# Kernel tuning notes

Hardware: AMD Instinct MI355X
Metric: run time of the kernel (lower is better)

## Reference

```python
import jax, jax.numpy as jnp
import numpy as np

B, L = 256, 8192
DIM, NPAT, HIST, WIN = 256, 64, 32, 8


def setup_inputs() -> dict:
    key = jax.random.key(0)
    ks = jax.random.split(key, 6)
    return {
        "x": jax.random.normal(ks[0], (B, L), dtype=jnp.float32),
        "avg_init": jax.random.normal(ks[1], (B, NPAT), dtype=jnp.float32),
        "conv_w": jax.random.normal(ks[2], (DIM, 1, HIST), dtype=jnp.float32) * 0.1,
        "conv_b": jax.random.normal(ks[3], (DIM,), dtype=jnp.float32) * 0.1,
        "keys_w": jax.random.normal(ks[4], (NPAT, DIM), dtype=jnp.float32) * 0.1,
        "shapes_w": jax.random.normal(ks[5], (WIN, NPAT), dtype=jnp.float32) * 0.1,
    }


def reference(x, avg_init, conv_w, conv_b, keys_w, shapes_w):
    b, l = x.shape
    n_pat = keys_w.shape[0]
    hist = conv_w.shape[2]
    win = shapes_w.shape[0]

    # randn avg_scores, centered (module draws fresh randn each forward; we take it as input)
    avg0 = avg_init - jnp.mean(avg_init, axis=-1, keepdims=True)

    padded = jnp.pad(x, ((0, 0), (hist - 1, 0)))[:, None, :]  # [B,1,L+hist-1]
    out = jax.lax.conv_general_dilated(
        padded, conv_w, window_strides=(win,), padding="VALID",
        dimension_numbers=("NCH", "OIH", "NCH"))
    out = out + conv_b[None, :, None]                     # [B,dim,T]
    out = jnp.transpose(out, (2, 0, 1))                   # [T,B,dim]

    # relu6(keys(out)) -> attn scores [T,B,n_pat]
    scores = jnp.clip(jnp.einsum("tbd,pd->tbp", out, keys_w), 0.0, 6.0)

    # sequential balanced-routing scan over T with running average scores
    def step(avg, score):                                 # avg,score: [B,n_pat]
        idx = jnp.argmax(score - avg, axis=-1)
        prob = jax.nn.one_hot(idx, n_pat, dtype=score.dtype)
        return avg + prob - 1.0 / n_pat, prob

    _, probs = jax.lax.scan(step, avg0, scores)           # probs: [T,B,n_pat]
    probs = jnp.transpose(probs, (1, 0, 2))               # [B,T,n_pat]

    signal = jnp.einsum("btp,wp->btw", probs, shapes_w).reshape(b, -1)[:, :l]
    return jax.nn.relu(signal - x)
```

## Files before the change

kernel.cpp:

```cpp
#include <hip/hip_runtime.h>


constexpr int Bb = 256, Ll = 8192, DIMc = 256, NPAT = 64, HIST = 32, WINc = 8;
constexpr int Tt = Ll / WINc;
constexpr int TC = 32;
constexpr int NC = Tt / TC;
constexpr float CINV = 1.0f / 64.0f;

#define DPP_MAXF(m, ctrl, rmask)                                               \
  do {                                                                         \
    int _mi = __float_as_int(m);                                               \
    int _ti = __builtin_amdgcn_update_dpp(_mi, _mi, (ctrl), (rmask), 0xF, false); \
    (m) = fmaxf((m), __int_as_float(_ti));                                     \
  } while (0)

__global__ __launch_bounds__(256) void precompute_kernel(
    const float* __restrict__ conv_w, const float* __restrict__ conv_b,
    const float* __restrict__ keys_w, float* __restrict__ wsf) {
  __shared__ float part[8][32];
  __shared__ float bred[4];
  const int p = blockIdx.x;
  const int t = threadIdx.x;
  const int h = t & 31, g = t >> 5;
  const float* kwp = keys_w + (size_t)p * DIMc;

  float acc = 0.f;
#pragma unroll
  for (int dd = 0; dd < 32; ++dd) {
    int d = g * 32 + dd;
    acc = fmaf(kwp[d], conv_w[d * HIST + h], acc);
  }
  part[g][h] = acc;

  float bp = kwp[t] * conv_b[t];
#pragma unroll
  for (int off = 32; off; off >>= 1) bp += __shfl_down(bp, off);
  if ((t & 63) == 0) bred[t >> 6] = bp;
  __syncthreads();

  if (t < 32) {
    float s = 0.f;
#pragma unroll
    for (int gg = 0; gg < 8; ++gg) s += part[gg][t];
    wsf[(t >> 2) * (NPAT * 4) + p * 4 + (t & 3)] = s;
  } else if (t == 32) {
    wsf[NPAT * HIST + p] = (bred[0] + bred[1]) + (bred[2] + bred[3]);
  }
}

__global__ __launch_bounds__(256) void shaper_kernel(
    const float* __restrict__ x, const float* __restrict__ avg_init,
    const float* __restrict__ shapes_w, const float* __restrict__ wsf,
    float* __restrict__ out) {
  __shared__ __align__(16) float xpad[HIST - 1 + Ll + 1];
  __shared__ float scb[2][TC * NPAT];
  __shared__ int   idxb[Tt];
  __shared__ float shp[WINc * NPAT];

  const int b    = blockIdx.x;
  const int tid  = threadIdx.x;
  const int wid  = tid >> 6;
  const int lane = tid & 63;
  const float* xrow = x + (size_t)b * Ll;

  if (tid < HIST - 1) xpad[tid] = 0.f;
  {
    const float4* xv4 = (const float4*)xrow;
#pragma unroll
    for (int k = 0; k < 8; ++k) {
      int i4 = k * 256 + tid;
      float4 v = xv4[i4];
      float* dst = xpad + HIST - 1 + i4 * 4;
      dst[0] = v.x; dst[1] = v.y; dst[2] = v.z; dst[3] = v.w;
    }
  }
  for (int i = tid; i < WINc * NPAT; i += 256) shp[i] = shapes_w[i];

  float4 w2v[8];
  float  b2 = 0.f;
  if (wid > 0) {
    const float4* w2g = (const float4*)wsf;
#pragma unroll
    for (int h4 = 0; h4 < 8; ++h4) w2v[h4] = w2g[h4 * 64 + lane];
    b2 = wsf[NPAT * HIST + lane];
  }
  float av = 0.f;
  if (wid == 0) {
    const float* ai = avg_init + (size_t)b * NPAT;
    float s = 0.f;
    for (int j = 0; j < NPAT; ++j) s += ai[j];
    av = ai[lane] - s * (1.0f / NPAT);
  }
  __syncthreads();

  auto fill = [&](int c, float* __restrict__ sb) {
    int base = c * TC;
    for (int tl = wid - 1; tl < TC; tl += 3) {
      int t = base + tl;
      const float4* xw = (const float4*)(xpad + t * WINc);
      float acc = b2;
#pragma unroll
      for (int h4 = 0; h4 < 8; ++h4) {
        float4 xv = xw[h4];
        float4 wv = w2v[h4];
        acc = fmaf(xv.x, wv.x, acc);
        acc = fmaf(xv.y, wv.y, acc);
        acc = fmaf(xv.z, wv.z, acc);
        acc = fmaf(xv.w, wv.w, acc);
      }
      sb[tl * NPAT + lane] = fminf(fmaxf(acc, 0.f), 6.f);
    }
  };

  auto scan_chunk = [&](const float* __restrict__ sb, int tbase) {
    float r[TC];
#pragma unroll
    for (int i = 0; i < TC; ++i) r[i] = sb[i * NPAT + lane];
    float v = r[0] - av;
    int stash = 0;
#pragma unroll
    for (int i = 0; i < TC; ++i) {
      float t0 = av - CINV;
      float t1 = (av + 1.0f) - CINV;
      float vA = 0.f, vB = 0.f;
      if (i + 1 < TC) { vA = r[i + 1] - t0; vB = r[i + 1] - t1; }
      float m = v;
      DPP_MAXF(m, 0xB1, 0xF);
      DPP_MAXF(m, 0x4E, 0xF);
      DPP_MAXF(m, 0x141, 0xF);
      DPP_MAXF(m, 0x140, 0xF);
      DPP_MAXF(m, 0x142, 0xA);
      DPP_MAXF(m, 0x143, 0xC);
      float gmax = __int_as_float(
          __builtin_amdgcn_readlane(__float_as_int(m), 63));
      unsigned long long mk = __ballot(v == gmax);
      int winner = __ffsll(mk) - 1;
      stash = (lane == i) ? winner : stash;
      bool win = (lane == winner);
      av = win ? t1 : t0;
      if (i + 1 < TC) v = win ? vB : vA;
    }
    if (lane < TC) idxb[tbase + lane] = stash;
  };

  if (wid > 0) fill(0, scb[0]);
  __syncthreads();

  for (int c = 0; c < NC; ++c) {
    if (wid == 0) {
      scan_chunk(scb[c & 1], c * TC);
    } else if (c + 1 < NC) {
      fill(c + 1, scb[(c + 1) & 1]);
    }
    __syncthreads();
  }

  float4* outv = (float4*)(out + (size_t)b * Ll);
#pragma unroll
  for (int k = 0; k < 8; ++k) {
    int i4 = k * 256 + tid;
    int l0 = i4 * 4;
    int t  = l0 >> 3;
    int w0 = l0 & 7;
    int p  = idxb[t];
    float4 o;
    o.x = fmaxf(shp[(w0 + 0) * NPAT + p] - xpad[HIST - 1 + l0 + 0], 0.f);
    o.y = fmaxf(shp[(w0 + 1) * NPAT + p] - xpad[HIST - 1 + l0 + 1], 0.f);
    o.z = fmaxf(shp[(w0 + 2) * NPAT + p] - xpad[HIST - 1 + l0 + 2], 0.f);
    o.w = fmaxf(shp[(w0 + 3) * NPAT + p] - xpad[HIST - 1 + l0 + 3], 0.f);
    outv[i4] = o;
  }
}

extern "C" void kernel_launch(void* const* d_in, const int* in_sizes, int n_in,
                              void* d_out, int out_size, void* d_ws, size_t ws_size,
                              hipStream_t stream) {
  const float* x        = (const float*)d_in[0];
  const float* avg_init = (const float*)d_in[1];
  const float* conv_w   = (const float*)d_in[2];
  const float* conv_b   = (const float*)d_in[3];
  const float* keys_w   = (const float*)d_in[4];
  const float* shapes_w = (const float*)d_in[5];
  float* wsf = (float*)d_ws;

  precompute_kernel<<<NPAT, 256, 0, stream>>>(conv_w, conv_b, keys_w, wsf);
  shaper_kernel<<<Bb, 256, 0, stream>>>(x, avg_init, shapes_w, wsf,
                                        (float*)d_out);
}
```

Measured before the change: 186.7 us.

## Restructure routing scan with ordered-int keys and deferred winner selection

Converts the per-step argmax in the sequential routing scan to unsigned order-preserving integer keys and keeps two candidate keys per lane, one for the not-winner case and one for the previous winner. The max reduction now excludes the previous winner's lane, stops after the row-level DPP stages and combines four readlanes with scalar max. The winner's alternative key is fetched separately, which takes the argmax off the critical dependency chain that previously waited on the full cross-row reduction. It adds scalar readlanes and tie-break logic and must preserve exact first-index tie semantics.

```diff
diff --git a/kernel.cpp b/kernel.cpp
--- a/kernel.cpp
+++ b/kernel.cpp
@@ -7,11 +7,16 @@
 constexpr int NC = Tt / TC;
 constexpr float CINV = 1.0f / 64.0f;
 
-#define DPP_MAXF(m, ctrl, rmask)                                               \
+__device__ __forceinline__ unsigned ordkey(float v) {
+  int b = __float_as_int(v);
+  return (unsigned)(b ^ ((b >> 31) | 0x80000000));
+}
+
+#define DPP_MAXU(m, ctrl)                                                      \
   do {                                                                         \
-    int _mi = __float_as_int(m);                                               \
-    int _ti = __builtin_amdgcn_update_dpp(_mi, _mi, (ctrl), (rmask), 0xF, false); \
-    (m) = fmaxf((m), __int_as_float(_ti));                                     \
+    unsigned _t = (unsigned)__builtin_amdgcn_update_dpp(                       \
+        (int)(m), (int)(m), (ctrl), 0xF, 0xF, false);                          \
+    (m) = ((m) > _t) ? (m) : _t;                                               \
   } while (0)
 
 __global__ __launch_bounds__(256) void precompute_kernel(
@@ -84,12 +89,12 @@
     for (int h4 = 0; h4 < 8; ++h4) w2v[h4] = w2g[h4 * 64 + lane];
     b2 = wsf[NPAT * HIST + lane];
   }
-  float av = 0.f;
+  float av0 = 0.f;
   if (wid == 0) {
     const float* ai = avg_init + (size_t)b * NPAT;
     float s = 0.f;
     for (int j = 0; j < NPAT; ++j) s += ai[j];
-    av = ai[lane] - s * (1.0f / NPAT);
+    av0 = ai[lane] - s * (1.0f / NPAT);
   }
   __syncthreads();
 
@@ -112,33 +117,46 @@
     }
   };
 
+  int   wS = 64;
+  float t0 = av0, t1 = av0;
+
   auto scan_chunk = [&](const float* __restrict__ sb, int tbase) {
     float r[TC];
 #pragma unroll
     for (int i = 0; i < TC; ++i) r[i] = sb[i * NPAT + lane];
-    float v = r[0] - av;
+    unsigned keyA = ordkey(r[0] - t0);
+    unsigned keyB = ordkey(r[0] - t1);
     int stash = 0;
 #pragma unroll
     for (int i = 0; i < TC; ++i) {
-      float t0 = av - CINV;
-      float t1 = (av + 1.0f) - CINV;
-      float vA = 0.f, vB = 0.f;
-      if (i + 1 < TC) { vA = r[i + 1] - t0; vB = r[i + 1] - t1; }
-      float m = v;
-      DPP_MAXF(m, 0xB1, 0xF);
-      DPP_MAXF(m, 0x4E, 0xF);
-      DPP_MAXF(m, 0x141, 0xF);
-      DPP_MAXF(m, 0x140, 0xF);
-      DPP_MAXF(m, 0x142, 0xA);
-      DPP_MAXF(m, 0x143, 0xC);
-      float gmax = __int_as_float(
-          __builtin_amdgcn_readlane(__float_as_int(m), 63));
-      unsigned long long mk = __ballot(v == gmax);
-      int winner = __ffsll(mk) - 1;
-      stash = (lane == i) ? winner : stash;
-      bool win = (lane == winner);
-      av = win ? t1 : t0;
-      if (i + 1 < TC) v = win ? vB : vA;
+      bool isw = (lane == wS);
+      unsigned keym0 = isw ? 0u : keyA;
+      unsigned m = keym0;
+      DPP_MAXU(m, 0xB1);
+      DPP_MAXU(m, 0x4E);
+      DPP_MAXU(m, 0x141);
+      DPP_MAXU(m, 0x140);
+      unsigned m0 = (unsigned)__builtin_amdgcn_readlane((int)m, 15);
+      unsigned m1 = (unsigned)__builtin_amdgcn_readlane((int)m, 31);
+      unsigned m2 = (unsigned)__builtin_amdgcn_readlane((int)m, 47);
+      unsigned m3 = (unsigned)__builtin_amdgcn_readlane((int)m, 63);
+      unsigned ka = m0 > m1 ? m0 : m1;
+      unsigned kb = m2 > m3 ? m2 : m3;
+      unsigned K1 = ka > kb ? ka : kb;
+      unsigned KB = (unsigned)__builtin_amdgcn_readlane((int)keyB, wS);
+      unsigned long long bal = __ballot(keym0 == K1);
+      int I1 = __ffsll(bal) - 1;
+      int wnew = (KB > K1) ? wS : ((KB == K1) ? (wS < I1 ? wS : I1) : I1);
+
+      float av = isw ? t1 : t0;
+      t0 = av - CINV;
+      t1 = (av + 1.0f) - CINV;
+      if (i + 1 < TC) {
+        keyA = ordkey(r[i + 1] - t0);
+        keyB = ordkey(r[i + 1] - t1);
+      }
+      stash = (lane == i) ? wnew : stash;
+      wS = wnew;
     }
     if (lane < TC) idxb[tbase + lane] = stash;
   };
```

After: 202.6 us. +8.5%, slower.

## Restructure routing scan with top-2 lookahead to shorten serial argmax dependency

Applied to the files above, without the earlier changes.

Scores are pre-shifted by the initial average and a time-dependent constant, so the scan only tracks an integer count per lane. Each step computes a top-2 reduction over ordered-int keys plus ballot masks that do not depend on the previous step's winner. The winner is then resolved with cheap scalar bit logic on the previous winner, taking the cross-lane reduction off the serial critical path. Winners are packed into 64-bit scalar registers, and the per-row mean of avg_init is computed with a DPP reduction instead of a serial loop. Rewriting the float arithmetic this way risks small rounding differences in tie-breaking.

```diff
diff --git a/kernel.cpp b/kernel.cpp
--- a/kernel.cpp
+++ b/kernel.cpp
@@ -7,12 +7,34 @@
 constexpr int NC = Tt / TC;
 constexpr float CINV = 1.0f / 64.0f;
 
-#define DPP_MAXF(m, ctrl, rmask)                                               \
+__device__ __forceinline__ unsigned ordk(float v) {
+  int b = __float_as_int(v);
+  return (unsigned)(b ^ ((b >> 31) | 0x80000000));
+}
+
+#define DPPI(x, ctrl) \
+  ((unsigned)__builtin_amdgcn_update_dpp((int)(x), (int)(x), (ctrl), 0xF, 0xF, false))
+
+#define TOP2_STAGE(M, S, ctrl)                    \
+  do {                                            \
+    unsigned _Md = DPPI(M, ctrl);                 \
+    unsigned _Sd = DPPI(S, ctrl);                 \
+    unsigned _mn = (M) < _Md ? (M) : _Md;         \
+    (M) = (M) > _Md ? (M) : _Md;                  \
+    (S) = (S) > _Sd ? (S) : _Sd;                  \
+    (S) = (S) > _mn ? (S) : _mn;                  \
+  } while (0)
+
+#define DPP_ADDF(s, ctrl, rmask)                                               \
   do {                                                                         \
-    int _mi = __float_as_int(m);                                               \
-    int _ti = __builtin_amdgcn_update_dpp(_mi, _mi, (ctrl), (rmask), 0xF, false); \
-    (m) = fmaxf((m), __int_as_float(_ti));                                     \
+    int _si = __float_as_int(s);                                               \
+    int _ti = __builtin_amdgcn_update_dpp(_si, _si, (ctrl), (rmask), 0xF, false); \
+    (s) += __int_as_float(_ti);                                                \
   } while (0)
+
+struct BalSet {
+  unsigned long long E1, E2, GT, GE;
+};
 
 __global__ __launch_bounds__(256) void precompute_kernel(
     const float* __restrict__ conv_w, const float* __restrict__ conv_b,
@@ -76,6 +98,20 @@
   }
   for (int i = tid; i < WINc * NPAT; i += 256) shp[i] = shapes_w[i];
 
+  float av0 = 0.f;
+  {
+    float s = avg_init[(size_t)b * NPAT + lane];
+    float t = s;
+    DPP_ADDF(t, 0xB1, 0xF);
+    DPP_ADDF(t, 0x4E, 0xF);
+    DPP_ADDF(t, 0x141, 0xF);
+    DPP_ADDF(t, 0x140, 0xF);
+    DPP_ADDF(t, 0x142, 0xA);
+    DPP_ADDF(t, 0x143, 0xC);
+    float tot = __int_as_float(__builtin_amdgcn_readlane(__float_as_int(t), 63));
+    av0 = s - tot * CINV;
+  }
+
   float4 w2v[8];
   float  b2 = 0.f;
   if (wid > 0) {
@@ -83,13 +119,6 @@
 #pragma unroll
     for (int h4 = 0; h4 < 8; ++h4) w2v[h4] = w2g[h4 * 64 + lane];
     b2 = wsf[NPAT * HIST + lane];
-  }
-  float av = 0.f;
-  if (wid == 0) {
-    const float* ai = avg_init + (size_t)b * NPAT;
-    float s = 0.f;
-    for (int j = 0; j < NPAT; ++j) s += ai[j];
-    av = ai[lane] - s * (1.0f / NPAT);
   }
   __syncthreads();
 
@@ -108,39 +137,87 @@
         acc = fmaf(xv.z, wv.z, acc);
         acc = fmaf(xv.w, wv.w, acc);
       }
-      sb[tl * NPAT + lane] = fminf(fmaxf(acc, 0.f), 6.f);
-    }
+      float sc = fminf(fmaxf(acc, 0.f), 6.f);
+      sb[tl * NPAT + lane] = (sc - av0) + (float)t * CINV;
+    }
+  };
+
+  float cnt = 0.f;
+  int   wp  = -1;
+  unsigned long long m_w = 0;
+  const float vone = 1.0f;
+
+  auto mkb = [&](float zv) {
+    BalSet B;
+    float z1 = zv - vone;
+    unsigned zu = ordk(zv);
+    unsigned M = zu, S = 0u;
+    TOP2_STAGE(M, S, 0xB1);
+    TOP2_STAGE(M, S, 0x4E);
+    TOP2_STAGE(M, S, 0x141);
+    TOP2_STAGE(M, S, 0x140);
+    unsigned M0 = (unsigned)__builtin_amdgcn_readlane((int)M, 0);
+    unsigned M1 = (unsigned)__builtin_amdgcn_readlane((int)M, 16);
+    unsigned M2 = (unsigned)__builtin_amdgcn_readlane((int)M, 32);
+    unsigned M3 = (unsigned)__builtin_amdgcn_readlane((int)M, 48);
+    unsigned S0 = (unsigned)__builtin_amdgcn_readlane((int)S, 0);
+    unsigned S1 = (unsigned)__builtin_amdgcn_readlane((int)S, 16);
+    unsigned S2 = (unsigned)__builtin_amdgcn_readlane((int)S, 32);
+    unsigned S3 = (unsigned)__builtin_amdgcn_readlane((int)S, 48);
+    unsigned h1 = M0 > M1 ? M0 : M1, l1 = M0 < M1 ? M0 : M1;
+    unsigned h2 = M2 > M3 ? M2 : M3, l2 = M2 < M3 ? M2 : M3;
+    unsigned Mu = h1 > h2 ? h1 : h2;
+    unsigned sa = h1 < h2 ? h1 : h2;
+    unsigned sb_ = l1 > l2 ? l1 : l2;
+    unsigned secM = sa > sb_ ? sa : sb_;
+    unsigned sr = S0 > S1 ? S0 : S1;
+    unsigned sr2 = S2 > S3 ? S2 : S3;
+    unsigned Smax = sr > sr2 ? sr : sr2;
+    unsigned Su = Smax > secM ? Smax : secM;
+    unsigned sbits = (Su >= 0x80000000u) ? (Su ^ 0x80000000u) : ~Su;
+    float Sf = __int_as_float((int)sbits);
+    B.E1 = __ballot(zu == Mu);
+    B.E2 = __ballot(zu == Su);
+    B.GT = __ballot(z1 > Sf);
+    B.GE = __ballot(z1 >= Sf);
+    return B;
   };
 
   auto scan_chunk = [&](const float* __restrict__ sb, int tbase) {
     float r[TC];
 #pragma unroll
     for (int i = 0; i < TC; ++i) r[i] = sb[i * NPAT + lane];
-    float v = r[0] - av;
-    int stash = 0;
+    unsigned long long sa0 = 0, sa1 = 0, sa2 = 0, sa3 = 0;
+    BalSet B = mkb(r[0] - cnt);
 #pragma unroll
     for (int i = 0; i < TC; ++i) {
-      float t0 = av - CINV;
-      float t1 = (av + 1.0f) - CINV;
-      float vA = 0.f, vB = 0.f;
-      if (i + 1 < TC) { vA = r[i + 1] - t0; vB = r[i + 1] - t1; }
-      float m = v;
-      DPP_MAXF(m, 0xB1, 0xF);
-      DPP_MAXF(m, 0x4E, 0xF);
-      DPP_MAXF(m, 0x141, 0xF);
-      DPP_MAXF(m, 0x140, 0xF);
-      DPP_MAXF(m, 0x142, 0xA);
-      DPP_MAXF(m, 0x143, 0xC);
-      float gmax = __int_as_float(
-          __builtin_amdgcn_readlane(__float_as_int(m), 63));
-      unsigned long long mk = __ballot(v == gmax);
-      int winner = __ffsll(mk) - 1;
-      stash = (lane == i) ? winner : stash;
-      bool win = (lane == winner);
-      av = win ? t1 : t0;
-      if (i + 1 < TC) v = win ? vB : vA;
-    }
-    if (lane < TC) idxb[tbase + lane] = stash;
+      unsigned long long b1x = B.E1 & ~m_w;
+      int jA  = __ffsll(b1x) - 1;
+      int jB1 = __ffsll(B.E2) - 1;
+      int wq  = wp & 63;
+      int gt  = (int)((B.GT >> wq) & 1);
+      int ge  = (int)((B.GE >> wq) & 1);
+      int jmn = wp < jB1 ? wp : jB1;
+      int wB  = gt ? wp : (ge ? jmn : jB1);
+      int w   = b1x ? jA : wB;
+      if (i < 10)      sa0 |= (unsigned long long)w << (6 * i);
+      else if (i < 20) sa1 |= (unsigned long long)w << (6 * (i - 10));
+      else if (i < 30) sa2 |= (unsigned long long)w << (6 * (i - 20));
+      else             sa3 |= (unsigned long long)w << (6 * (i - 30));
+      cnt += (lane == wp) ? 1.0f : 0.0f;
+      wp  = w;
+      m_w = 1ull << w;
+      if (i + 1 < TC) B = mkb(r[i + 1] - cnt);
+    }
+    cnt += (lane == wp) ? 1.0f : 0.0f;
+    wp  = -1;
+    m_w = 0;
+    unsigned long long src = (lane < 10) ? sa0 : (lane < 20) ? sa1
+                           : (lane < 30) ? sa2 : sa3;
+    int sh = 6 * (lane - ((lane < 10) ? 0 : (lane < 20) ? 10
+                          : (lane < 30) ? 20 : 30));
+    int widx = (int)((src >> sh) & 63);
+    if (lane < TC) idxb[tbase + lane] = widx;
   };
 
   if (wid > 0) fill(0, scb[0]);
```

Measured after the change: 261.8 us. 1.4x slower.

## Pack four patterns per lane in routing scan to shorten the argmax reduction

Applied to the files above, without the earlier changes.

The sequential routing scan now maps the 64 patterns onto 16 lanes with 4 patterns each, replicated across the four 16-lane rows. Each step does a local 4-way max plus 4 row-local DPP steps, which removes the cross-row DPP stages and the readlane from the serial critical path. The winner index is recovered from four ballots and a min, and the next chunk's score rows are prefetched as float4 loads in a rotating 3-register buffer. In exchange it adds extra ballots and selects per step. Exact ties would now mark several patterns as winners in the average update, which differs from the reference's first-index argmax.

```diff
diff --git a/kernel.cpp b/kernel.cpp
--- a/kernel.cpp
+++ b/kernel.cpp
@@ -7,10 +7,10 @@
 constexpr int NC = Tt / TC;
 constexpr float CINV = 1.0f / 64.0f;
 
-#define DPP_MAXF(m, ctrl, rmask)                                               \
+#define DPP_MAXF(m, ctrl)                                                      \
   do {                                                                         \
     int _mi = __float_as_int(m);                                               \
-    int _ti = __builtin_amdgcn_update_dpp(_mi, _mi, (ctrl), (rmask), 0xF, false); \
+    int _ti = __builtin_amdgcn_update_dpp(_mi, _mi, (ctrl), 0xF, 0xF, false);  \
     (m) = fmaxf((m), __int_as_float(_ti));                                     \
   } while (0)
 
@@ -53,7 +53,7 @@
     const float* __restrict__ shapes_w, const float* __restrict__ wsf,
     float* __restrict__ out) {
   __shared__ __align__(16) float xpad[HIST - 1 + Ll + 1];
-  __shared__ float scb[2][TC * NPAT];
+  __shared__ __align__(16) float scb[2][TC * NPAT];
   __shared__ int   idxb[Tt];
   __shared__ float shp[WINc * NPAT];
 
@@ -61,6 +61,7 @@
   const int tid  = threadIdx.x;
   const int wid  = tid >> 6;
   const int lane = tid & 63;
+  const int lq   = lane & 15;
   const float* xrow = x + (size_t)b * Ll;
 
   if (tid < HIST - 1) xpad[tid] = 0.f;
@@ -84,12 +85,14 @@
     for (int h4 = 0; h4 < 8; ++h4) w2v[h4] = w2g[h4 * 64 + lane];
     b2 = wsf[NPAT * HIST + lane];
   }
-  float av = 0.f;
+  float av[4] = {0.f, 0.f, 0.f, 0.f};
   if (wid == 0) {
     const float* ai = avg_init + (size_t)b * NPAT;
     float s = 0.f;
     for (int j = 0; j < NPAT; ++j) s += ai[j];
-    av = ai[lane] - s * (1.0f / NPAT);
+#pragma unroll
+    for (int k = 0; k < 4; ++k)
+      av[k] = ai[lq * 4 + k] - s * (1.0f / NPAT);
   }
   __syncthreads();
 
@@ -113,32 +116,59 @@
   };
 
   auto scan_chunk = [&](const float* __restrict__ sb, int tbase) {
-    float r[TC];
-#pragma unroll
-    for (int i = 0; i < TC; ++i) r[i] = sb[i * NPAT + lane];
-    float v = r[0] - av;
+    const float4* sb4 = (const float4*)sb;
+    float4 rr0 = sb4[0 * 16 + lq];
+    float4 rr1 = sb4[1 * 16 + lq];
+    float4 rr2 = sb4[2 * 16 + lq];
+    float v0 = rr0.x - av[0], v1 = rr0.y - av[1];
+    float v2 = rr0.z - av[2], v3 = rr0.w - av[3];
     int stash = 0;
 #pragma unroll
     for (int i = 0; i < TC; ++i) {
-      float t0 = av - CINV;
-      float t1 = (av + 1.0f) - CINV;
-      float vA = 0.f, vB = 0.f;
-      if (i + 1 < TC) { vA = r[i + 1] - t0; vB = r[i + 1] - t1; }
-      float m = v;
-      DPP_MAXF(m, 0xB1, 0xF);
-      DPP_MAXF(m, 0x4E, 0xF);
-      DPP_MAXF(m, 0x141, 0xF);
-      DPP_MAXF(m, 0x140, 0xF);
-      DPP_MAXF(m, 0x142, 0xA);
-      DPP_MAXF(m, 0x143, 0xC);
-      float gmax = __int_as_float(
-          __builtin_amdgcn_readlane(__float_as_int(m), 63));
-      unsigned long long mk = __ballot(v == gmax);
-      int winner = __ffsll(mk) - 1;
-      stash = (lane == i) ? winner : stash;
-      bool win = (lane == winner);
-      av = win ? t1 : t0;
-      if (i + 1 < TC) v = win ? vB : vA;
+      float4 nxt = (i % 3 == 0) ? rr1 : (i % 3 == 1) ? rr2 : rr0;
+      float T0[4], T1[4], VA[4], VB[4];
+#pragma unroll
+      for (int k = 0; k < 4; ++k) {
+        T0[k] = av[k] - CINV;
+        T1[k] = (av[k] + 1.0f) - CINV;
+      }
+      if (i + 1 < TC) {
+        VA[0] = nxt.x - T0[0]; VB[0] = nxt.x - T1[0];
+        VA[1] = nxt.y - T0[1]; VB[1] = nxt.y - T1[1];
+        VA[2] = nxt.z - T0[2]; VB[2] = nxt.z - T1[2];
+        VA[3] = nxt.w - T0[3]; VB[3] = nxt.w - T1[3];
+      }
+      if (i + 2 < TC) {
+        float4 ld = sb4[(i + 2) * 16 + lq];
+        if (i % 3 == 0) rr2 = ld; else if (i % 3 == 1) rr0 = ld; else rr1 = ld;
+      }
+      float m01 = fmaxf(v0, v1), m23 = fmaxf(v2, v3);
+      float m = fmaxf(m01, m23);
+      DPP_MAXF(m, 0xB1);
+      DPP_MAXF(m, 0x4E);
+      DPP_MAXF(m, 0x141);
+      DPP_MAXF(m, 0x140);
+      bool e0 = (v0 == m), e1 = (v1 == m), e2 = (v2 == m), e3 = (v3 == m);
+      av[0] = e0 ? T1[0] : T0[0];
+      av[1] = e1 ? T1[1] : T0[1];
+      av[2] = e2 ? T1[2] : T0[2];
+      av[3] = e3 ? T1[3] : T0[3];
+      if (i + 1 < TC) {
+        v0 = e0 ? VB[0] : VA[0];
+        v1 = e1 ? VB[1] : VA[1];
+        v2 = e2 ? VB[2] : VA[2];
+        v3 = e3 ? VB[3] : VA[3];
+      }
+      unsigned long long bl0 = __ballot(e0), bl1 = __ballot(e1);
+      unsigned long long bl2 = __ballot(e2), bl3 = __ballot(e3);
+      int c0 = bl0 ? (((__ffsll(bl0) - 1) & 15) << 2) + 0 : 999;
+      int c1 = bl1 ? (((__ffsll(bl1) - 1) & 15) << 2) + 1 : 999;
+      int c2 = bl2 ? (((__ffsll(bl2) - 1) & 15) << 2) + 2 : 999;
+      int c3 = bl3 ? (((__ffsll(bl3) - 1) & 15) << 2) + 3 : 999;
+      int cA = c0 < c1 ? c0 : c1;
+      int cB = c2 < c3 ? c2 : c3;
+      int w  = cA < cB ? cA : cB;
+      stash = (lane == i) ? w : stash;
     }
     if (lane < TC) idxb[tbase + lane] = stash;
   };
```

New measurement: 267.3 us. 1.43x slower.
